# Optimization experiments

Measured on AMD Instinct MI355X. Metric: run time of the kernel, lower is better.

## Reference

```python
import jax, jax.numpy as jnp
import numpy as np

C = 16  # number of classes (matches batch_ids fill_max)
XMIN, XMAX = 1e-37, 1.0 - 1e-5

def setup_inputs() -> dict:
    key = jax.random.key(0)
    k1, k2 = jax.random.split(key)
    hidden = jax.random.normal(k1, (65536, 512), dtype=jnp.float32)
    batch_ids = jax.random.randint(k2, (65536,), 0, C, dtype=jnp.int64)
    return {"hidden": hidden, "batch_ids": batch_ids, "d": 64}

def reference(hidden, batch_ids, d):
    N, D = hidden.shape
    seg = lambda v: jax.ops.segment_sum(v, batch_ids, num_segments=C)
    counts = seg(jnp.ones((N,), hidden.dtype))                  # [C]
    means = seg(hidden) / counts[:, None]                       # [C, D]
    # within-class sum of squared deviations, per feature dim
    withins = seg((hidden - means[batch_ids]) ** 2)             # [C, D]
    # pairwise: global mean of pair is (m_i+m_j)/2, so each class's between
    # term is ((m_i-m_j)/2)^2; weighted by counts it sums to that * (n_i+n_j)
    half_diff = (means[:, None, :] - means[None, :, :]) * 0.5   # [C, C, D]
    pair_counts = counts[:, None] + counts[None, :]             # [C, C]
    pair_between = half_diff * half_diff * pair_counts[:, :, None]
    pair_within = withins[:, None, :] + withins[None, :, :]
    d2 = pair_counts - 2.0
    d2 = jnp.where(d2 == 0.0, 1e-5, d2)
    x = pair_between / (pair_between + pair_within)
    x = jnp.clip(x, XMIN, XMAX)
    a = jnp.full_like(x, 0.5)                                   # d1/2
    b = jnp.broadcast_to((d2 * 0.5)[:, :, None], x.shape)       # d2/2
    xbetainc = jax.scipy.special.betainc(a, b, x)               # [C, C, D]
    top_k, _ = jax.lax.top_k(xbetainc, d)                       # [C, C, d]
    per_pair = jnp.sum(jnp.log(top_k), axis=-1)                 # [C, C]
    mask = jnp.triu(jnp.ones((C, C), dtype=bool), k=1)          # pairs i<j
    total = jnp.sum(jnp.where(mask, per_pair, jnp.zeros_like(per_pair)))
    return -total
```

## Files before the change

### kernel.cpp

```cpp
#include <hip/hip_runtime.h>
#include <math.h>

#define NUM_C 16
#define DIMS 512
#define SEG_ROWS 256
#define NREP 8

__device__ inline void atomAddF(float* p, float v) { unsafeAtomicAdd(p, v); }

__global__ __launch_bounds__(256) void k_counts(const int* __restrict__ bids,
                                                int* __restrict__ counts, int n) {
    __shared__ int hist[NUM_C];
    int tid = threadIdx.x;
    if (tid < NUM_C) hist[tid] = 0;
    __syncthreads();
    for (int i = blockIdx.x * 256 + tid; i < n; i += gridDim.x * 256)
        atomicAdd(&hist[bids[i]], 1);
    __syncthreads();
    if (tid < NUM_C) atomicAdd(&counts[tid], hist[tid]);
}

__global__ __launch_bounds__(256) void k_segsum(const float* __restrict__ hidden,
                                                const int* __restrict__ bids,
                                                float* __restrict__ gsum_rep,
                                                float* __restrict__ gsq_rep) {
    __shared__ float acc[NUM_C * 256 * 2];
    const int tid = threadIdx.x;
    const int g = blockIdx.x & 1;
    const int chunk = blockIdx.x >> 1;

    #pragma unroll
    for (int c = 0; c < NUM_C; ++c) {
        acc[(c * 256 + tid) * 2]     = 0.f;
        acc[(c * 256 + tid) * 2 + 1] = 0.f;
    }

    const int rowbase = chunk * SEG_ROWS;
    const float* hp = hidden + (size_t)rowbase * DIMS + g * 256 + tid;

    for (int it = 0; it < SEG_ROWS; it += 8) {
        int cs[8]; float vs[8];
        #pragma unroll
        for (int u = 0; u < 8; ++u) cs[u] = bids[rowbase + it + u];
        #pragma unroll
        for (int u = 0; u < 8; ++u) vs[u] = hp[(size_t)(it + u) * DIMS];
        #pragma unroll
        for (int u = 0; u < 8; ++u) {
            float2* slot = reinterpret_cast<float2*>(&acc[(cs[u] * 256 + tid) * 2]);
            float2 s = *slot;
            s.x += vs[u];
            s.y += vs[u] * vs[u];
            *slot = s;
        }
    }
    __syncthreads();

    const int rep = (blockIdx.x >> 1) & (NREP - 1);
    for (int s = tid; s < NUM_C * 256; s += 256) {
        const int c = s >> 8, l = s & 255;
        const int gdim = g * 256 + l;
        atomAddF(&gsum_rep[(size_t)rep * NUM_C * DIMS + c * DIMS + gdim], acc[s * 2]);
        atomAddF(&gsq_rep [(size_t)rep * NUM_C * DIMS + c * DIMS + gdim], acc[s * 2 + 1]);
    }
}

__global__ __launch_bounds__(256) void k_final(const float* __restrict__ gsum_rep,
                                               const float* __restrict__ gsq_rep,
                                               const int* __restrict__ counts,
                                               float* __restrict__ means,
                                               float* __restrict__ withins) {
    int idx = blockIdx.x * 256 + threadIdx.x;
    if (idx >= NUM_C * DIMS) return;
    float s = 0.f, q = 0.f;
    #pragma unroll
    for (int r = 0; r < NREP; ++r) {
        s += gsum_rep[r * NUM_C * DIMS + idx];
        q += gsq_rep [r * NUM_C * DIMS + idx];
    }
    int c = idx / DIMS;
    float n = (float)counts[c];
    float m = s / n;
    means[idx] = m;
    float w = q - s * s / n;
    withins[idx] = w > 0.f ? w : 0.f;
}

__device__ double betacf_d(double a, double b, double x) {
    const double FPMIN = 1e-300, EPS = 1e-15;
    double qab = a + b, qap = a + 1.0, qam = a - 1.0;
    double cc = 1.0, dd = 1.0 - qab * x / qap;
    if (fabs(dd) < FPMIN) dd = FPMIN;
    dd = 1.0 / dd;
    double h = dd;
    for (int m = 1; m <= 1000; ++m) {
        double m2 = 2.0 * m;
        double aa = m * (b - m) * x / ((qam + m2) * (a + m2));
        dd = 1.0 + aa * dd; if (fabs(dd) < FPMIN) dd = FPMIN;
        cc = 1.0 + aa / cc; if (fabs(cc) < FPMIN) cc = FPMIN;
        dd = 1.0 / dd;
        h *= dd * cc;
        aa = -(a + m) * (qab + m) * x / ((a + m2) * (qap + m2));
        dd = 1.0 + aa * dd; if (fabs(dd) < FPMIN) dd = FPMIN;
        cc = 1.0 + aa / cc; if (fabs(cc) < FPMIN) cc = FPMIN;
        dd = 1.0 / dd;
        double del = dd * cc;
        h *= del;
        if (fabs(del - 1.0) < EPS) break;
    }
    return h;
}

__device__ double betainc_reg(double a, double b, double x) {
    if (x <= 0.0) return 1e-300;
    if (x >= 1.0) return 1.0;
    double lnbt = lgamma(a + b) - lgamma(a) - lgamma(b) + a * log(x) + b * log1p(-x);
    double bt = exp(lnbt);
    double r;
    if (x < (a + 1.0) / (a + b + 2.0)) r = bt * betacf_d(a, b, x) / a;
    else                               r = 1.0 - bt * betacf_d(b, a, 1.0 - x) / b;
    if (r < 1e-300) r = 1e-300;
    if (r > 1.0) r = 1.0;
    return r;
}

__global__ __launch_bounds__(512) void k_pairs(const float* __restrict__ means,
                                               const float* __restrict__ withins,
                                               const int* __restrict__ counts,
                                               const int* __restrict__ dptr,
                                               float* __restrict__ out) {
    __shared__ float xs[DIMS];
    __shared__ double wsum[8];
    const int tid = threadIdx.x;

    int p = blockIdx.x, i = 0, rem = p;
    while (rem >= NUM_C - 1 - i) { rem -= NUM_C - 1 - i; ++i; }
    const int j = i + 1 + rem;

    const float ni = (float)counts[i], nj = (float)counts[j];
    const float pc = ni + nj;

    {
        float mi = means[i * DIMS + tid], mj = means[j * DIMS + tid];
        float hd = (mi - mj) * 0.5f;
        float between = hd * hd * pc;
        float within = withins[i * DIMS + tid] + withins[j * DIMS + tid];
        float x = between / (between + within);
        if (!(x >= 1e-37f)) x = 1e-37f;
        const float XM = 1.0f - 1e-5f;
        if (x > XM) x = XM;
        xs[tid] = x;
    }

    for (int kk = 2; kk <= DIMS; kk <<= 1) {
        for (int jj = kk >> 1; jj > 0; jj >>= 1) {
            __syncthreads();
            const int ixj = tid ^ jj;
            if (ixj > tid) {
                const float va = xs[tid], vb = xs[ixj];
                const bool sw = ((tid & kk) == 0) ? (va < vb) : (va > vb);
                if (sw) { xs[tid] = vb; xs[ixj] = va; }
            }
        }
    }
    __syncthreads();

    const int d = *dptr;
    double part = 0.0;
    if (tid < d) {
        double d2 = (double)pc - 2.0;
        if (d2 == 0.0) d2 = 1e-5;
        part = log(betainc_reg(0.5, d2 * 0.5, (double)xs[tid]));
    }
    for (int off = 32; off > 0; off >>= 1) part += __shfl_down(part, off, 64);
    if ((tid & 63) == 0) wsum[tid >> 6] = part;
    __syncthreads();
    if (tid == 0) {
        double t = 0.0;
        for (int w = 0; w < 8; ++w) t += wsum[w];
        atomAddF(out, (float)(-t));
    }
}

extern "C" void kernel_launch(void* const* d_in, const int* in_sizes, int n_in,
                              void* d_out, int out_size, void* d_ws, size_t ws_size,
                              hipStream_t stream) {
    const float* hidden = (const float*)d_in[0];
    const int* bids = (const int*)d_in[1];
    const int* dptr = (const int*)d_in[2];
    float* out = (float*)d_out;
    const int N = in_sizes[1];

    char* ws = (char*)d_ws;
    int* counts     = (int*)ws;
    float* gsum_rep = (float*)(ws + 256);
    float* gsq_rep  = (float*)(ws + 256 + NREP * NUM_C * DIMS * 4);
    float* means    = (float*)(ws + 256 + 2 * NREP * NUM_C * DIMS * 4);
    float* withins  = (float*)(ws + 256 + 2 * NREP * NUM_C * DIMS * 4 + NUM_C * DIMS * 4);

    hipMemsetAsync(d_ws, 0, 256 + 2 * NREP * NUM_C * DIMS * 4, stream);
    hipMemsetAsync(d_out, 0, sizeof(float), stream);

    k_counts<<<64, 256, 0, stream>>>(bids, counts, N);
    k_segsum<<<(N / SEG_ROWS) * 2, 256, 0, stream>>>(hidden, bids, gsum_rep, gsq_rep);
    k_final<<<(NUM_C * DIMS + 255) / 256, 256, 0, stream>>>(gsum_rep, gsq_rep, counts, means, withins);
    k_pairs<<<NUM_C * (NUM_C - 1) / 2, 512, 0, stream>>>(means, withins, counts, dptr, out);
}
```

Measured before the change: 258.9 us.

## Sort rows by class for segsum and replace double betainc with float Simpson quadrature

Adds a counting-sort pass (counts, prefix, scatter) so each segsum block gathers rows of a single class and accumulates in registers with float4 loads, instead of shared-memory histograms with replicated global atomics. The double-precision continued-fraction betainc is replaced by a float Simpson-rule integral in sqrt(x) space, with the beta normaliser taken from a Stirling-style approximation. Each integral is split across 8 lanes. This removes slow FP64 iterative work and shared-memory scatter traffic, at the cost of extra launches and accuracy that depends on the quadrature and on the approximation holding for large b.

```diff
diff --git a/kernel.cpp b/kernel.cpp
--- a/kernel.cpp
+++ b/kernel.cpp
@@ -3,124 +3,130 @@
 
 #define NUM_C 16
 #define DIMS 512
-#define SEG_ROWS 256
-#define NREP 8
+#define CHUNKS 32
 
 __device__ inline void atomAddF(float* p, float v) { unsafeAtomicAdd(p, v); }
 
 __global__ __launch_bounds__(256) void k_counts(const int* __restrict__ bids,
                                                 int* __restrict__ counts, int n) {
-    __shared__ int hist[NUM_C];
-    int tid = threadIdx.x;
-    if (tid < NUM_C) hist[tid] = 0;
-    __syncthreads();
-    for (int i = blockIdx.x * 256 + tid; i < n; i += gridDim.x * 256)
-        atomicAdd(&hist[bids[i]], 1);
-    __syncthreads();
-    if (tid < NUM_C) atomicAdd(&counts[tid], hist[tid]);
+    __shared__ int h[NUM_C];
+    const int tid = threadIdx.x;
+    if (tid < NUM_C) h[tid] = 0;
+    __syncthreads();
+    const int i0 = (blockIdx.x * 256 + tid) * 4;
+    if (i0 + 3 < n) {
+        int4 c4 = *reinterpret_cast<const int4*>(bids + i0);
+        atomicAdd(&h[c4.x], 1); atomicAdd(&h[c4.y], 1);
+        atomicAdd(&h[c4.z], 1); atomicAdd(&h[c4.w], 1);
+    }
+    __syncthreads();
+    if (tid < NUM_C) atomicAdd(&counts[tid], h[tid]);
+}
+
+__global__ void k_prefix(const int* __restrict__ counts,
+                         int* __restrict__ offs, int* __restrict__ gcur) {
+    if (threadIdx.x == 0) {
+        int acc = 0;
+        for (int c = 0; c < NUM_C; ++c) { offs[c] = acc; gcur[c] = acc; acc += counts[c]; }
+    }
+}
+
+__global__ __launch_bounds__(256) void k_scatter(const int* __restrict__ bids,
+                                                 int* __restrict__ gcur,
+                                                 int* __restrict__ perm, int n) {
+    __shared__ int lh[NUM_C], lb[NUM_C], lc[NUM_C];
+    const int tid = threadIdx.x;
+    if (tid < NUM_C) lh[tid] = 0;
+    __syncthreads();
+    const int i0 = (blockIdx.x * 256 + tid) * 4;
+    int4 c4 = make_int4(0, 0, 0, 0);
+    const bool ok = (i0 + 3 < n);
+    if (ok) {
+        c4 = *reinterpret_cast<const int4*>(bids + i0);
+        atomicAdd(&lh[c4.x], 1); atomicAdd(&lh[c4.y], 1);
+        atomicAdd(&lh[c4.z], 1); atomicAdd(&lh[c4.w], 1);
+    }
+    __syncthreads();
+    if (tid < NUM_C) { lb[tid] = atomicAdd(&gcur[tid], lh[tid]); lc[tid] = 0; }
+    __syncthreads();
+    if (ok) {
+        perm[lb[c4.x] + atomicAdd(&lc[c4.x], 1)] = i0;
+        perm[lb[c4.y] + atomicAdd(&lc[c4.y], 1)] = i0 + 1;
+        perm[lb[c4.z] + atomicAdd(&lc[c4.z], 1)] = i0 + 2;
+        perm[lb[c4.w] + atomicAdd(&lc[c4.w], 1)] = i0 + 3;
+    }
 }
 
 __global__ __launch_bounds__(256) void k_segsum(const float* __restrict__ hidden,
-                                                const int* __restrict__ bids,
-                                                float* __restrict__ gsum_rep,
-                                                float* __restrict__ gsq_rep) {
-    __shared__ float acc[NUM_C * 256 * 2];
-    const int tid = threadIdx.x;
-    const int g = blockIdx.x & 1;
-    const int chunk = blockIdx.x >> 1;
-
-    #pragma unroll
-    for (int c = 0; c < NUM_C; ++c) {
-        acc[(c * 256 + tid) * 2]     = 0.f;
-        acc[(c * 256 + tid) * 2 + 1] = 0.f;
-    }
-
-    const int rowbase = chunk * SEG_ROWS;
-    const float* hp = hidden + (size_t)rowbase * DIMS + g * 256 + tid;
-
-    for (int it = 0; it < SEG_ROWS; it += 8) {
-        int cs[8]; float vs[8];
-        #pragma unroll
-        for (int u = 0; u < 8; ++u) cs[u] = bids[rowbase + it + u];
-        #pragma unroll
-        for (int u = 0; u < 8; ++u) vs[u] = hp[(size_t)(it + u) * DIMS];
-        #pragma unroll
-        for (int u = 0; u < 8; ++u) {
-            float2* slot = reinterpret_cast<float2*>(&acc[(cs[u] * 256 + tid) * 2]);
-            float2 s = *slot;
-            s.x += vs[u];
-            s.y += vs[u] * vs[u];
-            *slot = s;
-        }
-    }
-    __syncthreads();
-
-    const int rep = (blockIdx.x >> 1) & (NREP - 1);
-    for (int s = tid; s < NUM_C * 256; s += 256) {
-        const int c = s >> 8, l = s & 255;
-        const int gdim = g * 256 + l;
-        atomAddF(&gsum_rep[(size_t)rep * NUM_C * DIMS + c * DIMS + gdim], acc[s * 2]);
-        atomAddF(&gsq_rep [(size_t)rep * NUM_C * DIMS + c * DIMS + gdim], acc[s * 2 + 1]);
-    }
-}
-
-__global__ __launch_bounds__(256) void k_final(const float* __restrict__ gsum_rep,
-                                               const float* __restrict__ gsq_rep,
+                                                const int* __restrict__ perm,
+                                                const int* __restrict__ counts,
+                                                const int* __restrict__ offs,
+                                                float* __restrict__ gsum,
+                                                float* __restrict__ gsq) {
+    const int tid = threadIdx.x;
+    const int c = blockIdx.x & (NUM_C - 1);
+    const int chunk = blockIdx.x >> 4;
+    const int cnt = counts[c];
+    const int base = offs[c];
+    const int len = (cnt + CHUNKS - 1) / CHUNKS;
+    const int lo = chunk * len;
+    const int hi = min(lo + len, cnt);
+    const int half = tid >> 7, ht = tid & 127;
+
+    float4 s = {0.f, 0.f, 0.f, 0.f}, q = {0.f, 0.f, 0.f, 0.f};
+#define LOADROW(r) (*(reinterpret_cast<const float4*>(hidden + (size_t)(r) * DIMS) + ht))
+#define ACC(v) { s.x += (v).x; s.y += (v).y; s.z += (v).z; s.w += (v).w; \
+                 q.x += (v).x*(v).x; q.y += (v).y*(v).y; q.z += (v).z*(v).z; q.w += (v).w*(v).w; }
+    int k = lo + half;
+    for (; k + 6 < hi; k += 8) {
+        const int r0 = perm[base + k],     r1 = perm[base + k + 2];
+        const int r2 = perm[base + k + 4], r3 = perm[base + k + 6];
+        const float4 v0 = LOADROW(r0), v1 = LOADROW(r1);
+        const float4 v2 = LOADROW(r2), v3 = LOADROW(r3);
+        ACC(v0); ACC(v1); ACC(v2); ACC(v3);
+    }
+    for (; k < hi; k += 2) {
+        const int r0 = perm[base + k];
+        const float4 v0 = LOADROW(r0);
+        ACC(v0);
+    }
+#undef LOADROW
+#undef ACC
+
+    __shared__ float red[128 * 8];
+    if (half == 1) {
+        float* p = &red[ht * 8];
+        p[0] = s.x; p[1] = s.y; p[2] = s.z; p[3] = s.w;
+        p[4] = q.x; p[5] = q.y; p[6] = q.z; p[7] = q.w;
+    }
+    __syncthreads();
+    if (half == 0) {
+        const float* p = &red[ht * 8];
+        s.x += p[0]; s.y += p[1]; s.z += p[2]; s.w += p[3];
+        q.x += p[4]; q.y += p[5]; q.z += p[6]; q.w += p[7];
+        float* gs = gsum + c * DIMS + 4 * ht;
+        float* gq = gsq  + c * DIMS + 4 * ht;
+        atomAddF(gs + 0, s.x); atomAddF(gs + 1, s.y);
+        atomAddF(gs + 2, s.z); atomAddF(gs + 3, s.w);
+        atomAddF(gq + 0, q.x); atomAddF(gq + 1, q.y);
+        atomAddF(gq + 2, q.z); atomAddF(gq + 3, q.w);
+    }
+}
+
+__global__ __launch_bounds__(256) void k_final(const float* __restrict__ gsum,
+                                               const float* __restrict__ gsq,
                                                const int* __restrict__ counts,
                                                float* __restrict__ means,
                                                float* __restrict__ withins) {
-    int idx = blockIdx.x * 256 + threadIdx.x;
+    const int idx = blockIdx.x * 256 + threadIdx.x;
     if (idx >= NUM_C * DIMS) return;
-    float s = 0.f, q = 0.f;
-    #pragma unroll
-    for (int r = 0; r < NREP; ++r) {
-        s += gsum_rep[r * NUM_C * DIMS + idx];
-        q += gsq_rep [r * NUM_C * DIMS + idx];
-    }
-    int c = idx / DIMS;
-    float n = (float)counts[c];
-    float m = s / n;
+    const int c = idx >> 9;
+    const float n = (float)counts[c];
+    const float s = gsum[idx];
+    const float m = s / n;
     means[idx] = m;
-    float w = q - s * s / n;
+    const float w = gsq[idx] - s * m;
     withins[idx] = w > 0.f ? w : 0.f;
-}
-
-__device__ double betacf_d(double a, double b, double x) {
-    const double FPMIN = 1e-300, EPS = 1e-15;
-    double qab = a + b, qap = a + 1.0, qam = a - 1.0;
-    double cc = 1.0, dd = 1.0 - qab * x / qap;
-    if (fabs(dd) < FPMIN) dd = FPMIN;
-    dd = 1.0 / dd;
-    double h = dd;
-    for (int m = 1; m <= 1000; ++m) {
-        double m2 = 2.0 * m;
-        double aa = m * (b - m) * x / ((qam + m2) * (a + m2));
-        dd = 1.0 + aa * dd; if (fabs(dd) < FPMIN) dd = FPMIN;
-        cc = 1.0 + aa / cc; if (fabs(cc) < FPMIN) cc = FPMIN;
-        dd = 1.0 / dd;
-        h *= dd * cc;
-        aa = -(a + m) * (qab + m) * x / ((a + m2) * (qap + m2));
-        dd = 1.0 + aa * dd; if (fabs(dd) < FPMIN) dd = FPMIN;
-        cc = 1.0 + aa / cc; if (fabs(cc) < FPMIN) cc = FPMIN;
-        dd = 1.0 / dd;
-        double del = dd * cc;
-        h *= del;
-        if (fabs(del - 1.0) < EPS) break;
-    }
-    return h;
-}
-
-__device__ double betainc_reg(double a, double b, double x) {
-    if (x <= 0.0) return 1e-300;
-    if (x >= 1.0) return 1.0;
-    double lnbt = lgamma(a + b) - lgamma(a) - lgamma(b) + a * log(x) + b * log1p(-x);
-    double bt = exp(lnbt);
-    double r;
-    if (x < (a + 1.0) / (a + b + 2.0)) r = bt * betacf_d(a, b, x) / a;
-    else                               r = 1.0 - bt * betacf_d(b, a, 1.0 - x) / b;
-    if (r < 1e-300) r = 1e-300;
-    if (r > 1.0) r = 1.0;
-    return r;
 }
 
 __global__ __launch_bounds__(512) void k_pairs(const float* __restrict__ means,
@@ -129,21 +135,20 @@
                                                const int* __restrict__ dptr,
                                                float* __restrict__ out) {
     __shared__ float xs[DIMS];
-    __shared__ double wsum[8];
+    __shared__ float wsum[8];
     const int tid = threadIdx.x;
 
     int p = blockIdx.x, i = 0, rem = p;
     while (rem >= NUM_C - 1 - i) { rem -= NUM_C - 1 - i; ++i; }
     const int j = i + 1 + rem;
 
-    const float ni = (float)counts[i], nj = (float)counts[j];
-    const float pc = ni + nj;
+    const float pc = (float)(counts[i] + counts[j]);
 
     {
-        float mi = means[i * DIMS + tid], mj = means[j * DIMS + tid];
-        float hd = (mi - mj) * 0.5f;
-        float between = hd * hd * pc;
-        float within = withins[i * DIMS + tid] + withins[j * DIMS + tid];
+        const float mi = means[i * DIMS + tid], mj = means[j * DIMS + tid];
+        const float hd = (mi - mj) * 0.5f;
+        const float between = hd * hd * pc;
+        const float within = withins[i * DIMS + tid] + withins[j * DIMS + tid];
         float x = between / (between + within);
         if (!(x >= 1e-37f)) x = 1e-37f;
         const float XM = 1.0f - 1e-5f;
@@ -165,19 +170,44 @@
     __syncthreads();
 
     const int d = *dptr;
-    double part = 0.0;
-    if (tid < d) {
-        double d2 = (double)pc - 2.0;
-        if (d2 == 0.0) d2 = 1e-5;
-        part = log(betainc_reg(0.5, d2 * 0.5, (double)xs[tid]));
+    float d2 = pc - 2.0f;
+    if (d2 == 0.0f) d2 = 1e-5f;
+    const float b = d2 * 0.5f;
+    const float bm1 = b - 1.0f;
+    const float invb = 1.0f / b;
+    const float ln2overB = 0.69314718f
+        - (0.5f * (1.14472989f - logf(b)) + log1pf(invb * (0.125f + 0.0078125f * invb)));
+
+    const int sub = tid & 7;
+    const int rounds = (d + 63) >> 6;
+    float part = 0.f;
+    for (int r = 0; r < rounds; ++r) {
+        const int q = (tid >> 3) + (r << 6);
+        const bool act = (q < d);
+        const float x = xs[act ? q : 0];
+        const float rt = sqrtf(x);
+        const float h = rt * (1.0f / 256.0f);
+        float acc = 0.f;
+        for (int k = sub; k <= 256; k += 8) {
+            const float sv = (float)k * h;
+            const float w = (k == 0 || k == 256) ? 1.f : ((k & 1) ? 4.f : 2.f);
+            acc += w * __expf(bm1 * log1pf(-sv * sv));
+        }
+        acc += __shfl_down(acc, 4, 64);
+        acc += __shfl_down(acc, 2, 64);
+        acc += __shfl_down(acc, 1, 64);
+        if (sub == 0 && act) {
+            float li = logf(acc * h * (1.0f / 3.0f)) + ln2overB;
+            part += (li < 0.f) ? li : 0.f;
+        }
     }
     for (int off = 32; off > 0; off >>= 1) part += __shfl_down(part, off, 64);
     if ((tid & 63) == 0) wsum[tid >> 6] = part;
     __syncthreads();
     if (tid == 0) {
-        double t = 0.0;
+        float t = 0.f;
         for (int w = 0; w < 8; ++w) t += wsum[w];
-        atomAddF(out, (float)(-t));
+        atomAddF(out, -t);
     }
 }
 
@@ -191,17 +221,23 @@
     const int N = in_sizes[1];
 
     char* ws = (char*)d_ws;
-    int* counts     = (int*)ws;
-    float* gsum_rep = (float*)(ws + 256);
-    float* gsq_rep  = (float*)(ws + 256 + NREP * NUM_C * DIMS * 4);
-    float* means    = (float*)(ws + 256 + 2 * NREP * NUM_C * DIMS * 4);
-    float* withins  = (float*)(ws + 256 + 2 * NREP * NUM_C * DIMS * 4 + NUM_C * DIMS * 4);
-
-    hipMemsetAsync(d_ws, 0, 256 + 2 * NREP * NUM_C * DIMS * 4, stream);
+    int* counts   = (int*)(ws + 0);
+    int* offs     = (int*)(ws + 256);
+    int* gcur     = (int*)(ws + 512);
+    float* gsum   = (float*)(ws + 1024);
+    float* gsq    = (float*)(ws + 33792);
+    float* means  = (float*)(ws + 66560);
+    float* withins= (float*)(ws + 99328);
+    int* perm     = (int*)(ws + 132096);
+
+    hipMemsetAsync(d_ws, 0, 66560, stream);
     hipMemsetAsync(d_out, 0, sizeof(float), stream);
 
-    k_counts<<<64, 256, 0, stream>>>(bids, counts, N);
-    k_segsum<<<(N / SEG_ROWS) * 2, 256, 0, stream>>>(hidden, bids, gsum_rep, gsq_rep);
-    k_final<<<(NUM_C * DIMS + 255) / 256, 256, 0, stream>>>(gsum_rep, gsq_rep, counts, means, withins);
-    k_pairs<<<NUM_C * (NUM_C - 1) / 2, 512, 0, stream>>>(means, withins, counts, dptr, out);
-}
+    const int nb = (N + 1023) / 1024;
+    k_counts <<<nb, 256, 0, stream>>>(bids, counts, N);
+    k_prefix <<<1, 64, 0, stream>>>(counts, offs, gcur);
+    k_scatter<<<nb, 256, 0, stream>>>(bids, gcur, perm, N);
+    k_segsum <<<NUM_C * CHUNKS, 256, 0, stream>>>(hidden, perm, counts, offs, gsum, gsq);
+    k_final  <<<(NUM_C * DIMS + 255) / 256, 256, 0, stream>>>(gsum, gsq, counts, means, withins);
+    k_pairs  <<<NUM_C * (NUM_C - 1) / 2, 512, 0, stream>>>(means, withins, counts, dptr, out);
+}
```

After: 237.9 us. 1.09x faster.
